# Kernel tuning notes

Hardware: AMD Instinct MI355X
Metric: run time of the kernel (lower is better)

Reference implementation:

```python
import jax, jax.numpy as jnp
import numpy as np


def setup_inputs() -> dict:
    key = jax.random.key(0)
    B, C, D, H, W = 8, 2, 128, 96, 128
    corr = jax.random.normal(key, (B, C, D, H, W), dtype=jnp.float32)
    return {"corr": corr, "maxdisp": 50, "is_ux": 1}


def reference(corr, maxdisp, is_ux):
    # corr: (B, C, D, H, W). For each pixel (i, j) and displacement dx in
    # [-maxdisp, maxdisp], linearly interpolate corr along the D axis at
    # position (j + dx) if is_ux else (i + dx), with zero padding outside
    # [0, D-1] (matches grid_sample bilinear, align_corners=True, H==1).
    B, C, D, H, W = corr.shape
    K = 2 * maxdisp + 1
    dx = jnp.linspace(-float(maxdisp), float(maxdisp), K)  # (K,)
    if is_ux:
        base = jnp.broadcast_to(jnp.arange(W, dtype=jnp.float32)[None, :], (H, W))
    else:
        base = jnp.broadcast_to(jnp.arange(H, dtype=jnp.float32)[:, None], (H, W))
    pos = base[None, :, :] + dx[:, None, None]           # (K, H, W)
    i0f = jnp.floor(pos)
    w1 = (pos - i0f).astype(corr.dtype)                  # lerp weight for upper tap
    i0 = i0f.astype(jnp.int32)
    i1 = i0 + 1
    m0 = ((i0 >= 0) & (i0 < D)).astype(corr.dtype)       # zero-padding masks
    m1 = ((i1 >= 0) & (i1 < D)).astype(corr.dtype)
    idx0 = jnp.clip(i0, 0, D - 1)[None, None]            # (1,1,K,H,W) -> broadcast
    idx1 = jnp.clip(i1, 0, D - 1)[None, None]
    g0 = jnp.take_along_axis(corr, idx0, axis=2)         # (B, C, K, H, W)
    g1 = jnp.take_along_axis(corr, idx1, axis=2)
    out = g0 * ((1.0 - w1) * m0)[None, None] + g1 * (w1 * m1)[None, None]
    return out  # (B, C, 2*maxdisp+1, H, W)
```

## Files before the change

kernel.cpp:

```cpp
#include <hip/hip_runtime.h>


#define B_ 8
#define C_ 2
#define D_ 128
#define H_ 96
#define W_ 128
#define NTHREADS 256

__global__ __launch_bounds__(NTHREADS) void corr2cost_kernel(
    const float* __restrict__ corr,
    const int* __restrict__ maxdisp_p,
    const int* __restrict__ isux_p,
    float* __restrict__ out) {
  __shared__ float lds[D_ * W_];

  const int t   = threadIdx.x;
  const int bid = blockIdx.x;
  const int h   = bid % H_;
  const int bc  = bid / H_;
  const int HW  = H_ * W_;

  const float* __restrict__ src = corr + (size_t)bc * D_ * HW + (size_t)h * W_;
  const int n4 = D_ * W_ / 4;
#pragma unroll
  for (int i = t; i < n4; i += NTHREADS) {
    const int d  = i >> 5;
    const int w4 = i & 31;
    const float4 v = *reinterpret_cast<const float4*>(src + (size_t)d * HW + w4 * 4);
    *reinterpret_cast<float4*>(&lds[d * W_ + w4 * 4]) = v;
  }
  __syncthreads();

  const int maxdisp = *maxdisp_p;
  const int is_ux   = *isux_p;
  const int K       = 2 * maxdisp + 1;

  const int w    = t & (W_ - 1);
  const int k0   = t >> 7;
  const int base = is_ux ? w : h;

  float* __restrict__ dst = out + (size_t)bc * K * HW + (size_t)h * W_ + w;

  for (int k = k0; k < K; k += 2) {
    const float posf = (float)(base + k - maxdisp);
    const float i0f  = floorf(posf);
    const float w1   = posf - i0f;
    const int   i0   = (int)i0f;
    const int   i1   = i0 + 1;
    const float g0 = (i0 >= 0 && i0 < D_) ? lds[i0 * W_ + w] : 0.0f;
    const float g1 = (i1 >= 0 && i1 < D_) ? lds[i1 * W_ + w] : 0.0f;
    dst[(size_t)k * HW] = g0 * (1.0f - w1) + g1 * w1;
  }
}

extern "C" void kernel_launch(void* const* d_in, const int* in_sizes, int n_in,
                              void* d_out, int out_size, void* d_ws, size_t ws_size,
                              hipStream_t stream) {
  const float* corr    = (const float*)d_in[0];
  const int*   maxdisp = (const int*)d_in[1];
  const int*   is_ux   = (const int*)d_in[2];
  float*       out     = (float*)d_out;

  const int grid = B_ * C_ * H_;
  corr2cost_kernel<<<grid, NTHREADS, 0, stream>>>(corr, maxdisp, is_ux, out);
}
```

Measured before the change: 181.5 us.

## Tile W into 32-wide strips and load only the needed D range into LDS

```diff
diff --git a/kernel.cpp b/kernel.cpp
--- a/kernel.cpp
+++ b/kernel.cpp
@@ -6,50 +6,59 @@
 #define D_ 128
 #define H_ 96
 #define W_ 128
-#define NTHREADS 256
+#define WT 32
+#define NT 256
 
-__global__ __launch_bounds__(NTHREADS) void corr2cost_kernel(
+__global__ __launch_bounds__(NT, 8) void corr2cost_kernel(
     const float* __restrict__ corr,
     const int* __restrict__ maxdisp_p,
     const int* __restrict__ isux_p,
     float* __restrict__ out) {
-  __shared__ float lds[D_ * W_];
+  __shared__ float lds[D_ * WT];
 
   const int t   = threadIdx.x;
   const int bid = blockIdx.x;
-  const int h   = bid % H_;
-  const int bc  = bid / H_;
-  const int HW  = H_ * W_;
+  const int wt   = bid & (W_ / WT - 1);
+  const int rest = bid >> 2;
+  const int h    = rest % H_;
+  const int bc   = rest / H_;
+  const int w0   = wt * WT;
+  const int HW   = H_ * W_;
 
-  const float* __restrict__ src = corr + (size_t)bc * D_ * HW + (size_t)h * W_;
-  const int n4 = D_ * W_ / 4;
-#pragma unroll
-  for (int i = t; i < n4; i += NTHREADS) {
-    const int d  = i >> 5;
-    const int w4 = i & 31;
-    const float4 v = *reinterpret_cast<const float4*>(src + (size_t)d * HW + w4 * 4);
-    *reinterpret_cast<float4*>(&lds[d * W_ + w4 * 4]) = v;
+  const int m     = *maxdisp_p;
+  const int is_ux = *isux_p;
+  const int K     = 2 * m + 1;
+
+  int dlo = (is_ux ? w0 : h) - m;
+  int dhi = (is_ux ? w0 + WT - 1 : h) + m + 1;
+  dlo = dlo > 0 ? dlo : 0;
+  dhi = dhi < D_ - 1 ? dhi : D_ - 1;
+
+  const float* __restrict__ src =
+      corr + (size_t)bc * D_ * HW + (size_t)h * W_ + w0;
+  const int r0 = t >> 3;
+  const int c4 = (t & 7) * 4;
+  for (int r = dlo + r0; r <= dhi; r += 32) {
+    *reinterpret_cast<float4*>(&lds[(r - dlo) * WT + c4]) =
+        *reinterpret_cast<const float4*>(src + (size_t)r * HW + c4);
   }
   __syncthreads();
 
-  const int maxdisp = *maxdisp_p;
-  const int is_ux   = *isux_p;
-  const int K       = 2 * maxdisp + 1;
+  const int wi   = t & (WT - 1);
+  const int kg   = t >> 5;
+  const int base = is_ux ? (w0 + wi) : h;
 
-  const int w    = t & (W_ - 1);
-  const int k0   = t >> 7;
-  const int base = is_ux ? w : h;
+  float* __restrict__ dst =
+      out + (size_t)bc * K * HW + (size_t)h * W_ + w0 + wi;
 
-  float* __restrict__ dst = out + (size_t)bc * K * HW + (size_t)h * W_ + w;
-
-  for (int k = k0; k < K; k += 2) {
-    const float posf = (float)(base + k - maxdisp);
+  for (int k = kg; k < K; k += NT / WT) {
+    const float posf = (float)(base + k - m);
     const float i0f  = floorf(posf);
     const float w1   = posf - i0f;
     const int   i0   = (int)i0f;
     const int   i1   = i0 + 1;
-    const float g0 = (i0 >= 0 && i0 < D_) ? lds[i0 * W_ + w] : 0.0f;
-    const float g1 = (i1 >= 0 && i1 < D_) ? lds[i1 * W_ + w] : 0.0f;
+    const float g0 = (i0 >= 0 && i0 < D_) ? lds[(i0 - dlo) * WT + wi] : 0.0f;
+    const float g1 = (i1 >= 0 && i1 < D_) ? lds[(i1 - dlo) * WT + wi] : 0.0f;
     dst[(size_t)k * HW] = g0 * (1.0f - w1) + g1 * w1;
   }
 }
@@ -62,6 +71,6 @@
   const int*   is_ux   = (const int*)d_in[2];
   float*       out     = (float*)d_out;
 
-  const int grid = B_ * C_ * H_;
-  corr2cost_kernel<<<grid, NTHREADS, 0, stream>>>(corr, maxdisp, is_ux, out);
+  const int grid = B_ * C_ * H_ * (W_ / WT);
+  corr2cost_kernel<<<grid, NT, 0, stream>>>(corr, maxdisp, is_ux, out);
 }
```

New measurement: 174.7 us. 1.04x faster.
